# Optimization experiments

Hardware: AMD Instinct MI355X
Metric: run time of the kernel (lower is better)

The kernel has to match this reference:

```python
import jax, jax.numpy as jnp
import numpy as np

N = 50000      # nodes
E = 800000     # edges per meta-path
P = 3          # meta-paths
IN = 128       # in_size
H = 8          # heads
D = 32         # out_size per head
EMB = 128      # embedding_dim


def setup_inputs() -> dict:
    key = jax.random.key(0)
    ks = jax.random.split(key, 7)
    h = jax.random.normal(ks[0], (N, IN), jnp.float32)
    edge_index = jax.random.randint(ks[1], (P, 2, E), 0, N, dtype=jnp.int32)
    fc_w = jax.random.normal(ks[2], (P, IN, H * D), jnp.float32) * 0.05
    attn_l = jax.random.normal(ks[3], (P, H, D), jnp.float32) * 0.1
    attn_r = jax.random.normal(ks[4], (P, H, D), jnp.float32) * 0.1
    sem_w = jax.random.normal(ks[5], (P * H * D, EMB), jnp.float32) * 0.05
    sem_b = jnp.zeros((EMB,), jnp.float32)
    return {"h": h, "edge_index": edge_index, "fc_w": fc_w,
            "attn_l": attn_l, "attn_r": attn_r, "sem_w": sem_w, "sem_b": sem_b}


def _gat(h, W, al, ar, src, dst):
    # DGL GATConv (no bias/residual), eval mode (no dropout)
    feat = (h @ W).reshape(N, H, D)                      # (N,H,D)
    el = jnp.einsum('nhd,hd->nh', feat, al)              # (N,H)
    er = jnp.einsum('nhd,hd->nh', feat, ar)
    e = jax.nn.leaky_relu(el[src] + er[dst], negative_slope=0.2)  # (E,H)
    # edge softmax over incoming edges of each dst node
    m = jax.ops.segment_max(e, dst, num_segments=N)      # (N,H); -inf only for empty segs (never indexed)
    ex = jnp.exp(e - m[dst])
    den = jax.ops.segment_sum(ex, dst, num_segments=N)   # (N,H)
    a = ex / den[dst]                                    # (E,H)
    msg = feat[src] * a[..., None]                       # (E,H,D) gather + weight
    out = jax.ops.segment_sum(msg, dst, num_segments=N)  # (N,H,D) scatter-add
    return jax.nn.elu(out).reshape(N, H * D)             # flatten(1)


def reference(h, edge_index, fc_w, attn_l, attn_r, sem_w, sem_b):
    src = edge_index[:, 0]  # (P,E)
    dst = edge_index[:, 1]
    # run one GATConv per meta-path, vectorized over the meta-path axis
    z = jax.vmap(_gat, in_axes=(None, 0, 0, 0, 0, 0))(h, fc_w, attn_l, attn_r, src, dst)  # (P,N,H*D)
    z = jnp.transpose(z, (1, 0, 2)).reshape(N, P * H * D)  # stack(dim=1) then reshape [N,-1]
    return z @ sem_w + sem_b                                # SemanticAttention.project2
```

## Files before the change

kernel.cpp:

```cpp
#include <hip/hip_runtime.h>
#include <hip/hip_bf16.h>

#define N_NODES 50000
#define N_EDGES 800000
#define NPATH 3
#define NBKT 196
#define NBKT3 (NPATH * NBKT)
#define NCHUNKBLK 256
#define CHUNK 9375
#define A_STR 264

typedef __attribute__((ext_vector_type(8))) short short8;
typedef __attribute__((ext_vector_type(4))) float v4f;

__device__ __forceinline__ short f2bf(float v, float* back) {
  unsigned u = __float_as_uint(v);
  unsigned r = (u + 0x7FFFu + ((u >> 16) & 1u)) >> 16;
  *back = __uint_as_float(r << 16);
  return (short)r;
}

__device__ __forceinline__ float bflo(unsigned u) {
  return __uint_as_float(u << 16);
}
__device__ __forceinline__ float bfhi(unsigned u) {
  return __uint_as_float(u & 0xFFFF0000u);
}

__global__ __launch_bounds__(256) void blk_count_kernel(
    const int* __restrict__ ei, int* __restrict__ cntmat) {
  __shared__ int lcnt[NBKT3];
  const int t = threadIdx.x, blk = blockIdx.x;
  for (int j = t; j < NBKT3; j += 256) lcnt[j] = 0;
  __syncthreads();
  const int lo = blk * CHUNK, hi = lo + CHUNK;
  for (int idx = lo + t; idx < hi; idx += 256) {
    int p = idx / N_EDGES, e = idx - p * N_EDGES;
    int d = ei[p * 2 * N_EDGES + N_EDGES + e];
    atomicAdd(&lcnt[p * NBKT + (d >> 8)], 1);
  }
  __syncthreads();
  for (int j = t; j < NBKT3; j += 256) cntmat[blk * NBKT3 + j] = lcnt[j];
}

__global__ __launch_bounds__(256) void col_scan_kernel(
    const int* __restrict__ cntmat, int* __restrict__ pos, int* __restrict__ btot) {
  __shared__ int tmp[256];
  const int b = blockIdx.x, t = threadIdx.x;
  int v = cntmat[t * NBKT3 + b];
  tmp[t] = v;
  __syncthreads();
  for (int ofs = 1; ofs < 256; ofs <<= 1) {
    int x = (t >= ofs) ? tmp[t - ofs] : 0;
    __syncthreads();
    tmp[t] += x;
    __syncthreads();
  }
  pos[b * 256 + t] = tmp[t] - v;
  if (t == 255) btot[b] = tmp[255];
}

__global__ __launch_bounds__(1024) void bucket_scan_kernel(
    const int* __restrict__ btot, int* __restrict__ boff) {
  __shared__ int tmp[1024];
  const int t = threadIdx.x;
  int v = (t < NBKT3) ? btot[t] : 0;
  tmp[t] = v;
  __syncthreads();
  for (int ofs = 1; ofs < 1024; ofs <<= 1) {
    int x = (t >= ofs) ? tmp[t - ofs] : 0;
    __syncthreads();
    tmp[t] += x;
    __syncthreads();
  }
  if (t < NBKT3) boff[t] = tmp[t] - v;
}

__global__ __launch_bounds__(256) void scatter_det_kernel(
    const int* __restrict__ ei, const int* __restrict__ boff,
    const int* __restrict__ pos, int2* __restrict__ ebuf) {
  __shared__ int cursor[NBKT3];
  const int t = threadIdx.x, blk = blockIdx.x;
  for (int j = t; j < NBKT3; j += 256)
    cursor[j] = boff[j] + pos[j * 256 + blk];
  __syncthreads();
  const int lo = blk * CHUNK, hi = lo + CHUNK;
  for (int idx = lo + t; idx < hi; idx += 256) {
    int p = idx / N_EDGES, e = idx - p * N_EDGES;
    int s = ei[p * 2 * N_EDGES + e];
    int d = ei[p * 2 * N_EDGES + N_EDGES + e];
    int ps = atomicAdd(&cursor[p * NBKT + (d >> 8)], 1);
    ebuf[ps] = make_int2(s, d);
  }
}

__global__ __launch_bounds__(256) void bucket_csr_kernel(
    const int2* __restrict__ ebuf, const int* __restrict__ boff,
    const int* __restrict__ btot,
    int* __restrict__ off3, int* __restrict__ deg3, int* __restrict__ csr_src) {
  __shared__ int cnt[256], excl[256], cur[256];
  const int b = blockIdx.x;
  const int t = threadIdx.x;
  const int p = b / NBKT;
  const int node_base = (b - p * NBKT) * 256;
  const int start = boff[b];
  const int ecount = btot[b];

  cnt[t] = 0;
  __syncthreads();
  for (int i = t; i < ecount; i += 256)
    atomicAdd(&cnt[ebuf[start + i].y & 255], 1);
  __syncthreads();

  int v = cnt[t];
  excl[t] = v;
  __syncthreads();
  for (int ofs = 1; ofs < 256; ofs <<= 1) {
    int x = (t >= ofs) ? excl[t - ofs] : 0;
    __syncthreads();
    excl[t] += x;
    __syncthreads();
  }
  int my_excl = excl[t] - v;
  cur[t] = my_excl;
  const int node = node_base + t;
  if (node < N_NODES) {
    off3[p * N_NODES + node] = start + my_excl;
    deg3[p * N_NODES + node] = v;
  }
  __syncthreads();

  for (int i = t; i < ecount; i += 256) {
    int2 e = ebuf[start + i];
    int pos2 = atomicAdd(&cur[e.y & 255], 1);
    csr_src[start + pos2] = e.x;
  }
}

__global__ __launch_bounds__(256) void prep_kernel(
    const float* __restrict__ fc_w, const float* __restrict__ attn_l,
    const float* __restrict__ attn_r, const float* __restrict__ sem_w,
    __hip_bfloat16* __restrict__ Wf_hi, __hip_bfloat16* __restrict__ Wf_lo,
    __hip_bfloat16* __restrict__ Bs_hi, __hip_bfloat16* __restrict__ Bs_lo) {
  const int p = blockIdx.x / 33;
  const int unit = blockIdx.x % 33;
  const int t = threadIdx.x;
  if (unit < 17) {
    const float* W = fc_w + (size_t)p * 128 * 256;
    int idx = unit * 256 + t;
    int lane = idx & 63;
    int tmp = idx >> 6;
    int nt = tmp % 17, kc = tmp / 17;
    int l15 = lane & 15, quad = lane >> 4;
    __hip_bfloat16* oh = Wf_hi + (size_t)p * 34816;
    __hip_bfloat16* ol = Wf_lo + (size_t)p * 34816;
    for (int j = 0; j < 8; j++) {
      int k = kc * 32 + quad * 8 + j;
      float v;
      if (nt < 16) {
        v = W[k * 256 + nt * 16 + l15];
      } else {
        int h8 = l15 & 7;
        const float* av = ((l15 < 8) ? attn_l : attn_r) + (size_t)p * 256 + h8 * 32;
        v = 0.f;
        for (int dd = 0; dd < 32; dd++)
          v = fmaf(W[k * 256 + h8 * 32 + dd], av[dd], v);
      }
      float back, back2;
      short hb = f2bf(v, &back);
      short lb = f2bf(v - back, &back2);
      ((short*)oh)[(tmp * 64 + lane) * 8 + j] = hb;
      ((short*)ol)[(tmp * 64 + lane) * 8 + j] = lb;
    }
  } else {
    const float* Ws = sem_w + (size_t)p * 256 * 128;
    int idx = (unit - 17) * 256 + t;
    int lane = idx & 63;
    int tmp = idx >> 6;
    int nt = tmp & 7, kc = tmp >> 3;
    int l15 = lane & 15, quad = lane >> 4;
    __hip_bfloat16* oh = Bs_hi + (size_t)p * 32768;
    __hip_bfloat16* ol = Bs_lo + (size_t)p * 32768;
    for (int j = 0; j < 8; j++) {
      int k = kc * 32 + quad * 8 + j;
      float v = Ws[k * 128 + nt * 16 + l15];
      float back, back2;
      short hb = f2bf(v, &back);
      short lb = f2bf(v - back, &back2);
      ((short*)oh)[(tmp * 64 + lane) * 8 + j] = hb;
      ((short*)ol)[(tmp * 64 + lane) * 8 + j] = lb;
    }
  }
}

__global__ __launch_bounds__(64) void feat_mfma_kernel(
    const float* __restrict__ h,
    const __hip_bfloat16* __restrict__ Wf_hi_all,
    const __hip_bfloat16* __restrict__ Wf_lo_all,
    __hip_bfloat16* __restrict__ feat3, float* __restrict__ el3,
    float* __restrict__ er3) {
  const int p = blockIdx.y;
  const __hip_bfloat16* Wf_hi = Wf_hi_all + (size_t)p * 34816;
  const __hip_bfloat16* Wf_lo = Wf_lo_all + (size_t)p * 34816;
  __hip_bfloat16* feat = feat3 + (size_t)p * N_NODES * 256;
  float* el = el3 + (size_t)p * N_NODES * 8;
  float* er = er3 + (size_t)p * N_NODES * 8;

  const int lane = threadIdx.x;
  const int l15 = lane & 15, quad = lane >> 4;
  const int m0 = blockIdx.x * 16;
  const int mrow = m0 + l15;

  v4f acc[17];
#pragma unroll
  for (int nt = 0; nt < 17; nt++) acc[nt] = {0.f, 0.f, 0.f, 0.f};

#pragma unroll
  for (int kc = 0; kc < 4; kc++) {
    const float* hrow = h + (size_t)mrow * 128 + kc * 32 + quad * 8;
    float4 fa = *(const float4*)hrow;
    float4 fb = *(const float4*)(hrow + 4);
    float fv[8] = {fa.x, fa.y, fa.z, fa.w, fb.x, fb.y, fb.z, fb.w};
    short8 ahi, alo;
#pragma unroll
    for (int q = 0; q < 8; q++) {
      float back, back2;
      ahi[q] = f2bf(fv[q], &back);
      alo[q] = f2bf(fv[q] - back, &back2);
    }
#pragma unroll
    for (int nt = 0; nt < 17; nt++) {
      const int o = ((kc * 17 + nt) * 64 + lane) * 8;
      short8 bhi = *(const short8*)(Wf_hi + o);
      short8 blo = *(const short8*)(Wf_lo + o);
      acc[nt] = __builtin_amdgcn_mfma_f32_16x16x32_bf16(ahi, bhi, acc[nt], 0, 0, 0);
      acc[nt] = __builtin_amdgcn_mfma_f32_16x16x32_bf16(ahi, blo, acc[nt], 0, 0, 0);
      acc[nt] = __builtin_amdgcn_mfma_f32_16x16x32_bf16(alo, bhi, acc[nt], 0, 0, 0);
    }
  }

#pragma unroll
  for (int nt = 0; nt < 16; nt++)
#pragma unroll
    for (int r = 0; r < 4; r++) {
      int m = m0 + quad * 4 + r;
      feat[(size_t)m * 256 + nt * 16 + l15] = __float2bfloat16(acc[nt][r]);
    }
#pragma unroll
  for (int r = 0; r < 4; r++) {
    int m = m0 + quad * 4 + r;
    float v = acc[16][r];
    if (l15 < 8) el[m * 8 + l15] = v;
    else         er[m * 8 + (l15 - 8)] = v;
  }
}

__global__ __launch_bounds__(512) void agg_sem_kernel(
    const int* __restrict__ csr_src, const int* __restrict__ off,
    const int* __restrict__ deg,
    const float* __restrict__ el, const float* __restrict__ er,
    const __hip_bfloat16* __restrict__ feat,
    const __hip_bfloat16* __restrict__ Bs_hi, const __hip_bfloat16* __restrict__ Bs_lo,
    const float* __restrict__ bias, float* __restrict__ out, int mode) {
  __shared__ __align__(16) short Ahi[16 * A_STR];
  __shared__ __align__(16) short Alo[16 * A_STR];
  const int t = threadIdx.x;
  const int w = t >> 6, lane = t & 63;
  const int half = lane >> 5;
  const int l5 = lane & 31;
  const int hh = l5 >> 2;
  const int node_base = blockIdx.x * 16;
  const ushort* fp = (const ushort*)feat;
  const ushort* fpl = fp + l5 * 8;
  const float* elh = el + hh;

#pragma unroll
  for (int i = 0; i < 2; i++) {
    const int node = node_base + 2 * w + i;
    const int n = deg[node];
    const int* lst = csr_src + off[node] + half;
    const float erh = er[node * 8 + hh];

    float aN[8] = {0.f, 0.f, 0.f, 0.f, 0.f, 0.f, 0.f, 0.f};
    float aD = 0.f;
    int j = 0;
    for (; j + 8 <= n; j += 8) {
      int s0 = lst[j + 0], s1 = lst[j + 2], s2 = lst[j + 4], s3 = lst[j + 6];
      unsigned u0 = (unsigned)s0, u1 = (unsigned)s1,
               u2 = (unsigned)s2, u3 = (unsigned)s3;
      float x0 = elh[(size_t)u0 * 8], x1 = elh[(size_t)u1 * 8],
            x2 = elh[(size_t)u2 * 8], x3 = elh[(size_t)u3 * 8];
      uint4 f0 = *(const uint4*)(fpl + (size_t)u0 * 256);
      uint4 f1 = *(const uint4*)(fpl + (size_t)u1 * 256);
      uint4 f2 = *(const uint4*)(fpl + (size_t)u2 * 256);
      uint4 f3 = *(const uint4*)(fpl + (size_t)u3 * 256);
#pragma unroll
      for (int u = 0; u < 4; u++) {
        float x = (u == 0) ? x0 : (u == 1) ? x1 : (u == 2) ? x2 : x3;
        uint4 f = (u == 0) ? f0 : (u == 1) ? f1 : (u == 2) ? f2 : f3;
        float xx = x + erh;
        xx = xx > 0.f ? xx : 0.2f * xx;
        float e = __expf(xx);
        aD += e;
        aN[0] = fmaf(e, bflo(f.x), aN[0]);
        aN[1] = fmaf(e, bfhi(f.x), aN[1]);
        aN[2] = fmaf(e, bflo(f.y), aN[2]);
        aN[3] = fmaf(e, bfhi(f.y), aN[3]);
        aN[4] = fmaf(e, bflo(f.z), aN[4]);
        aN[5] = fmaf(e, bfhi(f.z), aN[5]);
        aN[6] = fmaf(e, bflo(f.w), aN[6]);
        aN[7] = fmaf(e, bfhi(f.w), aN[7]);
      }
    }
    for (; j < n; j += 2) {
      int v = (j + half) < n;
      int s_ = lst[v ? j : j - 1];
      unsigned su = (unsigned)s_;
      float x = elh[(size_t)su * 8];
      uint4 f = *(const uint4*)(fpl + (size_t)su * 256);
      float xx = x + erh;
      xx = xx > 0.f ? xx : 0.2f * xx;
      float e = v ? __expf(xx) : 0.f;
      aD += e;
      aN[0] = fmaf(e, bflo(f.x), aN[0]);
      aN[1] = fmaf(e, bfhi(f.x), aN[1]);
      aN[2] = fmaf(e, bflo(f.y), aN[2]);
      aN[3] = fmaf(e, bfhi(f.y), aN[3]);
      aN[4] = fmaf(e, bflo(f.z), aN[4]);
      aN[5] = fmaf(e, bfhi(f.z), aN[5]);
      aN[6] = fmaf(e, bflo(f.w), aN[6]);
      aN[7] = fmaf(e, bfhi(f.w), aN[7]);
    }

#pragma unroll
    for (int k = 0; k < 8; k++) aN[k] += __shfl_xor(aN[k], 32, 64);
    aD += __shfl_xor(aD, 32, 64);

    float inv = (n > 0) ? 1.f / aD : 0.f;
    short8 hi8, lo8;
#pragma unroll
    for (int k = 0; k < 8; k++) {
      float r = aN[k] * inv;
      r = r > 0.f ? r : (__expf(r) - 1.f);
      float back, back2;
      hi8[k] = f2bf(r, &back);
      lo8[k] = f2bf(r - back, &back2);
    }
    const int row = 2 * w + i;
    short* dst = half ? Alo : Ahi;
    short8 vv = half ? lo8 : hi8;
    *(short8*)&dst[row * A_STR + l5 * 8] = vv;
  }
  __syncthreads();

  const int nt = w;
  const int l15 = lane & 15, quad = lane >> 4;
  v4f acc = {0.f, 0.f, 0.f, 0.f};
#pragma unroll
  for (int kc = 0; kc < 8; kc++) {
    short8 ahi = *(const short8*)&Ahi[l15 * A_STR + kc * 32 + quad * 8];
    short8 alo = *(const short8*)&Alo[l15 * A_STR + kc * 32 + quad * 8];
    const int o = ((kc * 8 + nt) * 64 + lane) * 8;
    short8 bhi = *(const short8*)(Bs_hi + o);
    short8 blo = *(const short8*)(Bs_lo + o);
    acc = __builtin_amdgcn_mfma_f32_16x16x32_bf16(ahi, bhi, acc, 0, 0, 0);
    acc = __builtin_amdgcn_mfma_f32_16x16x32_bf16(ahi, blo, acc, 0, 0, 0);
    acc = __builtin_amdgcn_mfma_f32_16x16x32_bf16(alo, bhi, acc, 0, 0, 0);
  }

#pragma unroll
  for (int r = 0; r < 4; r++) {
    int m = node_base + quad * 4 + r;
    size_t o = (size_t)m * 128 + nt * 16 + l15;
    float v = acc[r];
    if (mode == 0) v += bias[nt * 16 + l15];
    else           v += out[o];
    out[o] = v;
  }
}

extern "C" void kernel_launch(void* const* d_in, const int* in_sizes, int n_in,
                              void* d_out, int out_size, void* d_ws, size_t ws_size,
                              hipStream_t stream) {
  const float* h      = (const float*)d_in[0];
  const int*   ei     = (const int*)d_in[1];
  const float* fc_w   = (const float*)d_in[2];
  const float* attn_l = (const float*)d_in[3];
  const float* attn_r = (const float*)d_in[4];
  const float* sem_w  = (const float*)d_in[5];
  const float* sem_b  = (const float*)d_in[6];
  float* out = (float*)d_out;

  char* ws = (char*)d_ws;
  __hip_bfloat16* feat3 = (__hip_bfloat16*)ws;
  float* el3     = (float*)(ws + 76800000);
  float* er3     = (float*)(ws + 81600000);
  int*   csr_src = (int*)(ws + 86400000);
  int2*  ebuf    = (int2*)(ws + 96000000);
  int*   deg3    = (int*)(ws + 115200000);
  int*   off3    = (int*)(ws + 115800000);
  int*   cntmat  = (int*)(ws + 116400000);
  int*   posm    = (int*)(ws + 117050000);
  int*   btot    = (int*)(ws + 117700000);
  int*   boff    = (int*)(ws + 117710000);
  __hip_bfloat16* Wf_hi = (__hip_bfloat16*)(ws + 117800000);
  __hip_bfloat16* Wf_lo = (__hip_bfloat16*)(ws + 118050000);
  __hip_bfloat16* Bs_hi = (__hip_bfloat16*)(ws + 118300000);
  __hip_bfloat16* Bs_lo = (__hip_bfloat16*)(ws + 118550000);

  blk_count_kernel<<<NCHUNKBLK, 256, 0, stream>>>(ei, cntmat);
  col_scan_kernel<<<NBKT3, 256, 0, stream>>>(cntmat, posm, btot);
  bucket_scan_kernel<<<1, 1024, 0, stream>>>(btot, boff);
  scatter_det_kernel<<<NCHUNKBLK, 256, 0, stream>>>(ei, boff, posm, ebuf);
  bucket_csr_kernel<<<NBKT3, 256, 0, stream>>>(ebuf, boff, btot, off3, deg3, csr_src);
  prep_kernel<<<NPATH * 33, 256, 0, stream>>>(fc_w, attn_l, attn_r, sem_w,
                                              Wf_hi, Wf_lo, Bs_hi, Bs_lo);

  feat_mfma_kernel<<<dim3(N_NODES / 16, NPATH), 64, 0, stream>>>(
      h, Wf_hi, Wf_lo, feat3, el3, er3);

  for (int p = 0; p < NPATH; p++) {
    agg_sem_kernel<<<N_NODES / 16, 512, 0, stream>>>(
        csr_src, off3 + p * N_NODES, deg3 + p * N_NODES,
        el3 + (size_t)p * N_NODES * 8, er3 + (size_t)p * N_NODES * 8,
        feat3 + (size_t)p * N_NODES * 256,
        Bs_hi + (size_t)p * 32768, Bs_lo + (size_t)p * 32768,
        sem_b, out, p);
  }
}
```

Baseline: 501.3 us.

## Fuse meta-path loop into one aggregation kernel with prefetched neighbor indices

Merges the three per-meta-path aggregation launches into one kernel that loops over paths and keeps the semantic-projection accumulator in registers. This removes the read-modify-write of the output between launches and two launch overheads. Neighbor indices for the first 64 edges are staged in shared memory and the gathers are software-pipelined one step ahead to hide latency. In exchange it adds two block barriers per path, more register pressure, and a fallback loop for nodes with more than 64 edges.

Result: faster. 477.6 us (-4.7%).

```diff
diff --git a/kernel.cpp b/kernel.cpp
--- a/kernel.cpp
+++ b/kernel.cpp
@@ -256,126 +256,169 @@
 }
 
 __global__ __launch_bounds__(512) void agg_sem_kernel(
-    const int* __restrict__ csr_src, const int* __restrict__ off,
-    const int* __restrict__ deg,
-    const float* __restrict__ el, const float* __restrict__ er,
-    const __hip_bfloat16* __restrict__ feat,
+    const int* __restrict__ csr_src, const int* __restrict__ off3,
+    const int* __restrict__ deg3,
+    const float* __restrict__ el3, const float* __restrict__ er3,
+    const __hip_bfloat16* __restrict__ feat3,
     const __hip_bfloat16* __restrict__ Bs_hi, const __hip_bfloat16* __restrict__ Bs_lo,
-    const float* __restrict__ bias, float* __restrict__ out, int mode) {
+    const float* __restrict__ bias, float* __restrict__ out) {
   __shared__ __align__(16) short Ahi[16 * A_STR];
   __shared__ __align__(16) short Alo[16 * A_STR];
+  __shared__ int idxbuf[8 * 64];
   const int t = threadIdx.x;
   const int w = t >> 6, lane = t & 63;
   const int half = lane >> 5;
   const int l5 = lane & 31;
   const int hh = l5 >> 2;
   const int node_base = blockIdx.x * 16;
-  const ushort* fp = (const ushort*)feat;
-  const ushort* fpl = fp + l5 * 8;
-  const float* elh = el + hh;
-
-#pragma unroll
-  for (int i = 0; i < 2; i++) {
-    const int node = node_base + 2 * w + i;
-    const int n = deg[node];
-    const int* lst = csr_src + off[node] + half;
-    const float erh = er[node * 8 + hh];
-
-    float aN[8] = {0.f, 0.f, 0.f, 0.f, 0.f, 0.f, 0.f, 0.f};
-    float aD = 0.f;
-    int j = 0;
-    for (; j + 8 <= n; j += 8) {
-      int s0 = lst[j + 0], s1 = lst[j + 2], s2 = lst[j + 4], s3 = lst[j + 6];
-      unsigned u0 = (unsigned)s0, u1 = (unsigned)s1,
-               u2 = (unsigned)s2, u3 = (unsigned)s3;
-      float x0 = elh[(size_t)u0 * 8], x1 = elh[(size_t)u1 * 8],
-            x2 = elh[(size_t)u2 * 8], x3 = elh[(size_t)u3 * 8];
-      uint4 f0 = *(const uint4*)(fpl + (size_t)u0 * 256);
-      uint4 f1 = *(const uint4*)(fpl + (size_t)u1 * 256);
-      uint4 f2 = *(const uint4*)(fpl + (size_t)u2 * 256);
-      uint4 f3 = *(const uint4*)(fpl + (size_t)u3 * 256);
-#pragma unroll
-      for (int u = 0; u < 4; u++) {
-        float x = (u == 0) ? x0 : (u == 1) ? x1 : (u == 2) ? x2 : x3;
-        uint4 f = (u == 0) ? f0 : (u == 1) ? f1 : (u == 2) ? f2 : f3;
-        float xx = x + erh;
-        xx = xx > 0.f ? xx : 0.2f * xx;
-        float e = __expf(xx);
-        aD += e;
-        aN[0] = fmaf(e, bflo(f.x), aN[0]);
-        aN[1] = fmaf(e, bfhi(f.x), aN[1]);
-        aN[2] = fmaf(e, bflo(f.y), aN[2]);
-        aN[3] = fmaf(e, bfhi(f.y), aN[3]);
-        aN[4] = fmaf(e, bflo(f.z), aN[4]);
-        aN[5] = fmaf(e, bfhi(f.z), aN[5]);
-        aN[6] = fmaf(e, bflo(f.w), aN[6]);
-        aN[7] = fmaf(e, bfhi(f.w), aN[7]);
-      }
-    }
-    for (; j < n; j += 2) {
-      int v = (j + half) < n;
-      int s_ = lst[v ? j : j - 1];
-      unsigned su = (unsigned)s_;
-      float x = elh[(size_t)su * 8];
-      uint4 f = *(const uint4*)(fpl + (size_t)su * 256);
-      float xx = x + erh;
-      xx = xx > 0.f ? xx : 0.2f * xx;
-      float e = v ? __expf(xx) : 0.f;
-      aD += e;
-      aN[0] = fmaf(e, bflo(f.x), aN[0]);
-      aN[1] = fmaf(e, bfhi(f.x), aN[1]);
-      aN[2] = fmaf(e, bflo(f.y), aN[2]);
-      aN[3] = fmaf(e, bfhi(f.y), aN[3]);
-      aN[4] = fmaf(e, bflo(f.z), aN[4]);
-      aN[5] = fmaf(e, bfhi(f.z), aN[5]);
-      aN[6] = fmaf(e, bflo(f.w), aN[6]);
-      aN[7] = fmaf(e, bfhi(f.w), aN[7]);
-    }
-
-#pragma unroll
-    for (int k = 0; k < 8; k++) aN[k] += __shfl_xor(aN[k], 32, 64);
-    aD += __shfl_xor(aD, 32, 64);
-
-    float inv = (n > 0) ? 1.f / aD : 0.f;
-    short8 hi8, lo8;
-#pragma unroll
-    for (int k = 0; k < 8; k++) {
-      float r = aN[k] * inv;
-      r = r > 0.f ? r : (__expf(r) - 1.f);
-      float back, back2;
-      hi8[k] = f2bf(r, &back);
-      lo8[k] = f2bf(r - back, &back2);
-    }
-    const int row = 2 * w + i;
-    short* dst = half ? Alo : Ahi;
-    short8 vv = half ? lo8 : hi8;
-    *(short8*)&dst[row * A_STR + l5 * 8] = vv;
-  }
-  __syncthreads();
-
+  const int l15 = lane & 15, quad = lane >> 4;
   const int nt = w;
-  const int l15 = lane & 15, quad = lane >> 4;
+  const int ibase = w * 64 + 32 * half;
+
   v4f acc = {0.f, 0.f, 0.f, 0.f};
-#pragma unroll
-  for (int kc = 0; kc < 8; kc++) {
-    short8 ahi = *(const short8*)&Ahi[l15 * A_STR + kc * 32 + quad * 8];
-    short8 alo = *(const short8*)&Alo[l15 * A_STR + kc * 32 + quad * 8];
-    const int o = ((kc * 8 + nt) * 64 + lane) * 8;
-    short8 bhi = *(const short8*)(Bs_hi + o);
-    short8 blo = *(const short8*)(Bs_lo + o);
-    acc = __builtin_amdgcn_mfma_f32_16x16x32_bf16(ahi, bhi, acc, 0, 0, 0);
-    acc = __builtin_amdgcn_mfma_f32_16x16x32_bf16(ahi, blo, acc, 0, 0, 0);
-    acc = __builtin_amdgcn_mfma_f32_16x16x32_bf16(alo, bhi, acc, 0, 0, 0);
-  }
-
+
+  for (int p = 0; p < NPATH; p++) {
+    const int* offp = off3 + p * N_NODES;
+    const int* degp = deg3 + p * N_NODES;
+    const float* elh = el3 + (size_t)p * N_NODES * 8 + hh;
+    const float* erp = er3 + (size_t)p * N_NODES * 8;
+    const ushort* fpl = (const ushort*)(feat3 + (size_t)p * N_NODES * 256) + l5 * 8;
+
+#pragma unroll
+    for (int i = 0; i < 2; i++) {
+      const int node = node_base + 2 * w + i;
+      const int n = degp[node];
+      const int* lst2 = csr_src + offp[node];
+      const float erh = erp[node * 8 + hh];
+
+      {
+        int pos = 2 * l5 + half;
+        int sl = 0;
+        if (pos < n) sl = lst2[pos];
+        idxbuf[w * 64 + lane] = sl;
+      }
+      const int ncov = n < 64 ? n : 64;
+      const int nh = (ncov - half + 1) >> 1;
+      const int nmax = (ncov + 1) >> 1;
+
+      float aN[8] = {0.f, 0.f, 0.f, 0.f, 0.f, 0.f, 0.f, 0.f};
+      float aD = 0.f;
+
+      int2 idc = {0, 0};
+      float xac = 0.f, xbc = 0.f;
+      uint4 fac = {0, 0, 0, 0}, fbc = {0, 0, 0, 0};
+      if (nmax > 0) {
+        idc = *(const int2*)&idxbuf[ibase];
+        xac = elh[(size_t)(unsigned)idc.x * 8];
+        xbc = elh[(size_t)(unsigned)idc.y * 8];
+        fac = *(const uint4*)(fpl + (size_t)(unsigned)idc.x * 256);
+        fbc = *(const uint4*)(fpl + (size_t)(unsigned)idc.y * 256);
+      }
+      for (int k = 0; k < nmax; k += 2) {
+        int2 idn = {0, 0};
+        float xan = 0.f, xbn = 0.f;
+        uint4 fan = {0, 0, 0, 0}, fbn = {0, 0, 0, 0};
+        if (k + 2 < nmax) {
+          idn = *(const int2*)&idxbuf[ibase + k + 2];
+          xan = elh[(size_t)(unsigned)idn.x * 8];
+          xbn = elh[(size_t)(unsigned)idn.y * 8];
+          fan = *(const uint4*)(fpl + (size_t)(unsigned)idn.x * 256);
+          fbn = *(const uint4*)(fpl + (size_t)(unsigned)idn.y * 256);
+        }
+        {
+          float xx = xac + erh;
+          xx = xx > 0.f ? xx : 0.2f * xx;
+          float e = (k < nh) ? __expf(xx) : 0.f;
+          aD += e;
+          aN[0] = fmaf(e, bflo(fac.x), aN[0]);
+          aN[1] = fmaf(e, bfhi(fac.x), aN[1]);
+          aN[2] = fmaf(e, bflo(fac.y), aN[2]);
+          aN[3] = fmaf(e, bfhi(fac.y), aN[3]);
+          aN[4] = fmaf(e, bflo(fac.z), aN[4]);
+          aN[5] = fmaf(e, bfhi(fac.z), aN[5]);
+          aN[6] = fmaf(e, bflo(fac.w), aN[6]);
+          aN[7] = fmaf(e, bfhi(fac.w), aN[7]);
+        }
+        {
+          float xx = xbc + erh;
+          xx = xx > 0.f ? xx : 0.2f * xx;
+          float e = (k + 1 < nh) ? __expf(xx) : 0.f;
+          aD += e;
+          aN[0] = fmaf(e, bflo(fbc.x), aN[0]);
+          aN[1] = fmaf(e, bfhi(fbc.x), aN[1]);
+          aN[2] = fmaf(e, bflo(fbc.y), aN[2]);
+          aN[3] = fmaf(e, bfhi(fbc.y), aN[3]);
+          aN[4] = fmaf(e, bflo(fbc.z), aN[4]);
+          aN[5] = fmaf(e, bfhi(fbc.z), aN[5]);
+          aN[6] = fmaf(e, bflo(fbc.w), aN[6]);
+          aN[7] = fmaf(e, bfhi(fbc.w), aN[7]);
+        }
+        idc = idn; xac = xan; xbc = xbn; fac = fan; fbc = fbn;
+      }
+      if (n > 64) {
+        for (int j = 64; j < n; j += 2) {
+          int v = (j + half) < n;
+          int s_ = v ? lst2[j + half] : 0;
+          unsigned su = (unsigned)s_;
+          float x = elh[(size_t)su * 8];
+          uint4 f = *(const uint4*)(fpl + (size_t)su * 256);
+          float xx = x + erh;
+          xx = xx > 0.f ? xx : 0.2f * xx;
+          float e = v ? __expf(xx) : 0.f;
+          aD += e;
+          aN[0] = fmaf(e, bflo(f.x), aN[0]);
+          aN[1] = fmaf(e, bfhi(f.x), aN[1]);
+          aN[2] = fmaf(e, bflo(f.y), aN[2]);
+          aN[3] = fmaf(e, bfhi(f.y), aN[3]);
+          aN[4] = fmaf(e, bflo(f.z), aN[4]);
+          aN[5] = fmaf(e, bfhi(f.z), aN[5]);
+          aN[6] = fmaf(e, bflo(f.w), aN[6]);
+          aN[7] = fmaf(e, bfhi(f.w), aN[7]);
+        }
+      }
+
+#pragma unroll
+      for (int k = 0; k < 8; k++) aN[k] += __shfl_xor(aN[k], 32, 64);
+      aD += __shfl_xor(aD, 32, 64);
+
+      float inv = (n > 0) ? 1.f / aD : 0.f;
+      short8 hi8, lo8;
+#pragma unroll
+      for (int k = 0; k < 8; k++) {
+        float r = aN[k] * inv;
+        r = r > 0.f ? r : (__expf(r) - 1.f);
+        float back, back2;
+        hi8[k] = f2bf(r, &back);
+        lo8[k] = f2bf(r - back, &back2);
+      }
+      const int row = 2 * w + i;
+      short* dst = half ? Alo : Ahi;
+      short8 vv = half ? lo8 : hi8;
+      *(short8*)&dst[row * A_STR + l5 * 8] = vv;
+    }
+    __syncthreads();
+
+    const __hip_bfloat16* bh = Bs_hi + (size_t)p * 32768;
+    const __hip_bfloat16* bl = Bs_lo + (size_t)p * 32768;
+#pragma unroll
+    for (int kc = 0; kc < 8; kc++) {
+      short8 ahi = *(const short8*)&Ahi[l15 * A_STR + kc * 32 + quad * 8];
+      short8 alo = *(const short8*)&Alo[l15 * A_STR + kc * 32 + quad * 8];
+      const int o = ((kc * 8 + nt) * 64 + lane) * 8;
+      short8 bhi = *(const short8*)(bh + o);
+      short8 blo = *(const short8*)(bl + o);
+      acc = __builtin_amdgcn_mfma_f32_16x16x32_bf16(ahi, bhi, acc, 0, 0, 0);
+      acc = __builtin_amdgcn_mfma_f32_16x16x32_bf16(ahi, blo, acc, 0, 0, 0);
+      acc = __builtin_amdgcn_mfma_f32_16x16x32_bf16(alo, bhi, acc, 0, 0, 0);
+    }
+    __syncthreads();
+  }
+
+  const float bv = bias[nt * 16 + l15];
 #pragma unroll
   for (int r = 0; r < 4; r++) {
     int m = node_base + quad * 4 + r;
-    size_t o = (size_t)m * 128 + nt * 16 + l15;
-    float v = acc[r];
-    if (mode == 0) v += bias[nt * 16 + l15];
-    else           v += out[o];
-    out[o] = v;
+    out[(size_t)m * 128 + nt * 16 + l15] = acc[r] + bv;
   }
 }
 
@@ -419,12 +462,6 @@
   feat_mfma_kernel<<<dim3(N_NODES / 16, NPATH), 64, 0, stream>>>(
       h, Wf_hi, Wf_lo, feat3, el3, er3);
 
-  for (int p = 0; p < NPATH; p++) {
-    agg_sem_kernel<<<N_NODES / 16, 512, 0, stream>>>(
-        csr_src, off3 + p * N_NODES, deg3 + p * N_NODES,
-        el3 + (size_t)p * N_NODES * 8, er3 + (size_t)p * N_NODES * 8,
-        feat3 + (size_t)p * N_NODES * 256,
-        Bs_hi + (size_t)p * 32768, Bs_lo + (size_t)p * 32768,
-        sem_b, out, p);
-  }
-}
+  agg_sem_kernel<<<N_NODES / 16, 512, 0, stream>>>(
+      csr_src, off3, deg3, el3, er3, feat3, Bs_hi, Bs_lo, sem_b, out);
+}
```
